# Performance work log

Hardware: AMD Instinct MI355X
Metric: run time of the kernel (lower is better)

Reference implementation:

```python
import jax, jax.numpy as jnp
import numpy as np

DT = 0.05      # bsde.delta_t
EPS = 1e-6     # BatchNormalization epsilon


def _bn(x, gamma, beta):
    # training-mode batch norm: statistics over the batch axis
    m = jnp.mean(x, axis=0, keepdims=True)
    v = jnp.var(x, axis=0, keepdims=True)
    return (x - m) * jax.lax.rsqrt(v + EPS) * gamma + beta


def _subnet(x, g0, b0, W0, g1, b1, W1, g2, b2, W2, bias2, g3, b3):
    # bn -> (dense -> bn -> relu) x 2 -> dense(+bias) -> bn
    x = _bn(x, g0, b0)
    x = jax.nn.relu(_bn(x @ W0, g1, b1))
    x = jax.nn.relu(_bn(x @ W1, g2, b2))
    x = _bn(x @ W2 + bias2, g3, b3)
    return x


def setup_inputs() -> dict:
    key = jax.random.key(0)
    B, D, N, H = 8192, 100, 20, 110
    T = N - 1  # number of subnets
    ks = jax.random.split(key, 18)
    u = lambda k, s, lo, hi: jax.random.uniform(k, s, jnp.float32, lo, hi)
    s_dh = np.sqrt(2.0 / (D + H)).astype(np.float32)
    s_hh = np.sqrt(2.0 / (H + H)).astype(np.float32)
    s_hd = np.sqrt(2.0 / (H + D)).astype(np.float32)
    return {
        "dw": jax.random.normal(ks[0], (B, D, N), jnp.float32) * np.sqrt(DT).astype(np.float32),
        "x": jax.random.normal(ks[1], (B, D, N + 1), jnp.float32),
        "mean_y_input": jax.random.normal(ks[2], (N,), jnp.float32),
        "y_init": u(ks[3], (1,), 0.0, 1.0),
        "z_init": u(ks[4], (1, D), -0.1, 0.1),
        "gamma0": u(ks[5], (T, D), 0.1, 0.5),
        "beta0": 0.1 * jax.random.normal(ks[6], (T, D), jnp.float32),
        "W0": s_dh * jax.random.normal(ks[7], (T, D, H), jnp.float32),
        "gamma1": u(ks[8], (T, H), 0.1, 0.5),
        "beta1": 0.1 * jax.random.normal(ks[9], (T, H), jnp.float32),
        "W1": s_hh * jax.random.normal(ks[10], (T, H, H), jnp.float32),
        "gamma2": u(ks[11], (T, H), 0.1, 0.5),
        "beta2": 0.1 * jax.random.normal(ks[12], (T, H), jnp.float32),
        "W2": s_hd * jax.random.normal(ks[13], (T, H, D), jnp.float32),
        "bias2": jnp.zeros((T, D), jnp.float32),
        "gamma3": u(ks[14], (T, D), 0.1, 0.5),
        "beta3": 0.1 * jax.random.normal(ks[15], (T, D), jnp.float32),
    }


def reference(dw, x, mean_y_input, y_init, z_init, gamma0, beta0, W0,
              gamma1, beta1, W1, gamma2, beta2, W2, bias2, gamma3, beta3):
    B, D, N = dw.shape
    T = N - 1
    # z at step t+1 depends only on x[:, :, t+1] and subnet t -> compute all in parallel
    x_steps = jnp.moveaxis(x[:, :, 1:N], 2, 0)  # [T, B, D]
    z_all = jax.vmap(_subnet)(x_steps, gamma0, beta0, W0, gamma1, beta1, W1,
                              gamma2, beta2, W2, bias2, gamma3, beta3) / D  # [T, B, D]
    z0 = jnp.broadcast_to(z_init, (B, D))          # all_one_vec @ z_init
    zs = jnp.concatenate([z0[None], z_all], axis=0)  # [N, B, D] (z used at each update)
    dw_steps = jnp.moveaxis(dw, 2, 0)               # [N, B, D]
    y0 = jnp.ones((B, 1), dw.dtype) * y_init

    def step(y, zd):
        z, dwt = zd
        # f_tf(t, x, y, z) = sin(y) for the SineBM equation
        y_new = y - DT * jnp.sin(y) + jnp.sum(z * dwt, axis=1, keepdims=True)
        return y_new, jnp.mean(y_new)

    y_final, means = jax.lax.scan(step, y0, (zs, dw_steps))
    mean_y = jnp.concatenate([jnp.mean(y0)[None], means[:T]])  # length N
    return y_final, mean_y
```

## Files before the change

kernel.cpp:

```cpp
#include <hip/hip_runtime.h>

typedef unsigned short u16;
typedef unsigned int   u32;

#define BATCH  8192
#define DIM    100
#define HID    110
#define TSUB   19
#define NSTEP  20
#define KP     128
#define NPAD   112
#define BN_EPS 1e-6f
#define DT_C   0.05f

#define SAB  1024
#define SAR  (BATCH / SAB)
#define SLICES 32

#define A3P  101

typedef __bf16 v8bf __attribute__((ext_vector_type(8)));
typedef float  v4f  __attribute__((ext_vector_type(4)));
typedef u16    u16x4 __attribute__((ext_vector_type(4)));

__device__ __forceinline__ u16 f2bf(float f) {
    u32 u = __float_as_uint(f);
    return (u16)((u + 0x7fffu + ((u >> 16) & 1u)) >> 16);
}
__device__ __forceinline__ float bf2f(u16 h) {
    return __uint_as_float(((u32)h) << 16);
}
__device__ __forceinline__ void acc4(float4& s, float4& q, float4 v) {
    s.x += v.x; s.y += v.y; s.z += v.z; s.w += v.w;
    q.x += v.x * v.x; q.y += v.y * v.y; q.z += v.z * v.z; q.w += v.w * v.w;
}

__global__ void statsA(const float* __restrict__ x, float* __restrict__ part,
                       u32* __restrict__ xT32) {
    __shared__ u16 xls[SAR][2112];
    const int tid = threadIdx.x;
    const int b0 = blockIdx.x * SAR;
    float4 s0 = {0,0,0,0}, q0 = {0,0,0,0};
    float4 s1 = {0,0,0,0}, q1 = {0,0,0,0};
    float4 s2 = {0,0,0,0}, q2 = {0,0,0,0};
#pragma unroll
    for (int r = 0; r < SAR; r++) {
        const float4* row = (const float4*)(x + (size_t)(b0 + r) * 2100);
        float4 v0 = row[tid];
        float4 v1 = row[tid + 256];
        acc4(s0, q0, v0);
        acc4(s1, q1, v1);
        u16x4 p0 = { f2bf(v0.x), f2bf(v0.y), f2bf(v0.z), f2bf(v0.w) };
        u16x4 p1 = { f2bf(v1.x), f2bf(v1.y), f2bf(v1.z), f2bf(v1.w) };
        *(u16x4*)&xls[r][tid * 4]        = p0;
        *(u16x4*)&xls[r][1024 + tid * 4] = p1;
        if (tid < 13) {
            float4 v2 = row[tid + 512];
            acc4(s2, q2, v2);
            u16x4 p2 = { f2bf(v2.x), f2bf(v2.y), f2bf(v2.z), f2bf(v2.w) };
            *(u16x4*)&xls[r][2048 + tid * 4] = p2;
        }
    }
    float* ps = part + (size_t)blockIdx.x * 4200;
    *(float4*)&ps[tid * 4]               = s0;
    *(float4*)&ps[1024 + tid * 4]        = s1;
    *(float4*)&ps[2100 + tid * 4]        = q0;
    *(float4*)&ps[2100 + 1024 + tid * 4] = q1;
    if (tid < 13) {
        *(float4*)&ps[2048 + tid * 4]        = s2;
        *(float4*)&ps[2100 + 2048 + tid * 4] = q2;
    }
    __syncthreads();
    const int TOT = TSUB * SAR * (NPAD / 2);
    for (int i = tid; i < TOT; i += 256) {
        int w = i % (NPAD / 2);
        int seg = i / (NPAD / 2);
        int r = seg % SAR, t = seg / SAR;
        int d0 = w * 2;
        u32 v = 0;
        if (d0 < DIM) {
            u16 lo = xls[r][d0 * 21 + t + 1];
            u16 hi = (d0 + 1 < DIM) ? xls[r][(d0 + 1) * 21 + t + 1] : (u16)0;
            v = (u32)lo | ((u32)hi << 16);
        }
        xT32[((size_t)t * BATCH + b0 + r) * (NPAD / 2) + w] = v;
    }
}

__global__ void statsB(const float* __restrict__ part, float* __restrict__ out) {
    int gid = blockIdx.x * 256 + threadIdx.x;
    if (gid >= 4200 * SLICES) return;
    int slice = gid / 4200;
    int o = gid - slice * 4200;
    const float* p = part + (size_t)slice * (SAB / SLICES) * 4200 + o;
    float acc = 0.f;
#pragma unroll 4
    for (int i = 0; i < SAB / SLICES; i++) acc += p[(size_t)i * 4200];
    atomicAdd(&out[o], acc);
}

__global__ void wtrans(const float* __restrict__ W0, const float* __restrict__ W1,
                       const float* __restrict__ W2, u16* __restrict__ WTsw) {
    __shared__ float lw[HID * HID];
    const int t = blockIdx.x, l = blockIdx.y, tid = threadIdx.x;
    const float* W; int K, N;
    if (l == 0)      { W = W0; K = DIM; N = HID; }
    else if (l == 1) { W = W1; K = HID; N = HID; }
    else             { W = W2; K = HID; N = DIM; }
    const float* Wt = W + (size_t)t * K * N;
    for (int i = tid; i < K * N; i += 256) lw[i] = Wt[i];
    __syncthreads();
    u16* out = WTsw + ((size_t)l * TSUB + t) * (NPAD * KP);
    for (int i = tid; i < NPAD * 16; i += 256) {
        int n = i / 16, p = i % 16;
        int kc = p ^ (n & 7);
        u16 o8[8];
#pragma unroll
        for (int j = 0; j < 8; j++) {
            int k = kc * 8 + j;
            float v = (k < K && n < N) ? lw[k * N + n] : 0.f;
            o8[j] = f2bf(v);
        }
        *(uint4*)&out[(size_t)n * KP + p * 8] = *(uint4*)o8;
    }
}

template <int KREAL, int NOUT, int IDXMODE, int RELU>
__global__ void gemm_kernel(const u16* __restrict__ Ain,
                            const u16* __restrict__ WTswL,
                            const float* __restrict__ sumIn,
                            const float* __restrict__ sqIn,
                            const float* __restrict__ gIn,
                            const float* __restrict__ bIn,
                            u16* __restrict__ Hout,
                            float* __restrict__ sumArr,
                            float* __restrict__ sqArr) {
    __shared__ __align__(16) u16 Alds[128 * KP];
    __shared__ __align__(16) u16 Blds[NPAD * KP];
    __shared__ float s_sum[NPAD], s_sq[NPAD];
    __shared__ float aAffL[KP], cAffL[KP];

    const int tid = threadIdx.x;
    const int mt = blockIdx.x;
    const int t  = blockIdx.y;
    const int brow0 = mt * 128;

    if (tid < NPAD) { s_sum[tid] = 0.f; s_sq[tid] = 0.f; }
    if (tid < KREAL) {
        int idx = (IDXMODE == 0) ? (tid * 21 + (t + 1)) : (t * KREAL + tid);
        float m = sumIn[idx] * (1.f / BATCH);
        float v = sqIn[idx] * (1.f / BATCH) - m * m;
        float rstd = rsqrtf(v + BN_EPS);
        float ga = gIn[t * KREAL + tid] * rstd;
        aAffL[tid] = ga;
        cAffL[tid] = bIn[t * KREAL + tid] - m * ga;
    }

    {
        const uint4* wsrc = (const uint4*)(WTswL + (size_t)t * NPAD * KP);
        uint4* bl = (uint4*)Blds;
#pragma unroll
        for (int i = 0; i < 7; i++) bl[tid + i * 256] = wsrc[tid + i * 256];
    }
    const int NCH = (KREAL + 7) / 8;
    for (int i = tid; i < 128 * (16 - NCH); i += 256) {
        int row = i / (16 - NCH);
        int kc  = NCH + i % (16 - NCH);
        uint4 z = {0, 0, 0, 0};
        *(uint4*)&Alds[row * KP + (kc ^ (row & 7)) * 8] = z;
    }
    __syncthreads();

    for (int cidx = tid; cidx < 128 * NCH; cidx += 256) {
        int row = cidx / NCH;
        int kc  = cidx % NCH;
        int k0  = kc * 8;
        const u16* hrow = Ain + ((size_t)t * BATCH + brow0 + row) * NPAD + k0;
        u16 hv[8];
        *(uint4*)hv = *(const uint4*)hrow;
        u16 pk[8];
#pragma unroll
        for (int j = 0; j < 8; j++) {
            int k = k0 + j;
            float av = (k < KREAL) ? fmaf(bf2f(hv[j]), aAffL[k], cAffL[k]) : 0.f;
            if (RELU) av = fmaxf(av, 0.f);
            pk[j] = f2bf(av);
        }
        *(uint4*)&Alds[row * KP + ((kc ^ (row & 7)) * 8)] = *(uint4*)pk;
    }
    __syncthreads();

    const int lane = tid & 63;
    const int wv   = tid >> 6;
    const int r0   = lane & 15;
    const int q    = lane >> 4;
    const int moff = wv * 32;

    v4f acc[2][7];
#pragma unroll
    for (int i = 0; i < 2; i++)
#pragma unroll
        for (int j = 0; j < 7; j++) { v4f z = {0.f, 0.f, 0.f, 0.f}; acc[i][j] = z; }

#pragma unroll
    for (int ks = 0; ks < 4; ks++) {
        int cbase = ks * 4 + q;
        v8bf afr[2];
#pragma unroll
        for (int mf = 0; mf < 2; mf++) {
            int row = moff + mf * 16 + r0;
            afr[mf] = *(const v8bf*)&Alds[row * KP + ((cbase ^ (row & 7)) * 8)];
        }
#pragma unroll
        for (int nf = 0; nf < 7; nf++) {
            int nr = nf * 16 + r0;
            v8bf bfr = *(const v8bf*)&Blds[nr * KP + ((cbase ^ (nr & 7)) * 8)];
            acc[0][nf] = __builtin_amdgcn_mfma_f32_16x16x32_bf16(afr[0], bfr, acc[0][nf], 0, 0, 0);
            acc[1][nf] = __builtin_amdgcn_mfma_f32_16x16x32_bf16(afr[1], bfr, acc[1][nf], 0, 0, 0);
        }
    }

#pragma unroll
    for (int mf = 0; mf < 2; mf++) {
#pragma unroll
        for (int nf = 0; nf < 7; nf++) {
            int n = nf * 16 + r0;
#pragma unroll
            for (int rg = 0; rg < 4; rg++) {
                int grow = brow0 + moff + mf * 16 + q * 4 + rg;
                Hout[((size_t)t * BATCH + grow) * NPAD + n] = f2bf(acc[mf][nf][rg]);
            }
        }
    }
#pragma unroll
    for (int nf = 0; nf < 7; nf++) {
        float cs = 0.f, cq = 0.f;
#pragma unroll
        for (int mf = 0; mf < 2; mf++)
#pragma unroll
            for (int rg = 0; rg < 4; rg++) {
                float vv = acc[mf][nf][rg];
                cs += vv; cq += vv * vv;
            }
        cs += __shfl_xor(cs, 16); cs += __shfl_xor(cs, 32);
        cq += __shfl_xor(cq, 16); cq += __shfl_xor(cq, 32);
        if (q == 0) {
            atomicAdd(&s_sum[nf * 16 + r0], cs);
            atomicAdd(&s_sq[nf * 16 + r0], cq);
        }
    }
    __syncthreads();
    if (tid < NOUT) {
        atomicAdd(&sumArr[t * NOUT + tid], s_sum[tid]);
        atomicAdd(&sqArr[t * NOUT + tid], s_sq[tid]);
    }
}

__global__ __launch_bounds__(256, 4)
void scan_kernel(const float* __restrict__ dw,
                 const u16* __restrict__ zbuf,
                 const float* __restrict__ sum3, const float* __restrict__ sq3,
                 const float* __restrict__ g3, const float* __restrict__ b3,
                 const float* __restrict__ z_init, const float* __restrict__ y_init,
                 float* __restrict__ yout, float* __restrict__ meanout) {
    __shared__ float a3l[TSUB * A3P], c3l[TSUB * A3P];
    __shared__ float bsum[NSTEP];
    const int tid = threadIdx.x;
    for (int i = tid; i < TSUB * DIM; i += 256) {
        int t = i / DIM, d = i - t * DIM;
        float m = sum3[i] * (1.f / BATCH);
        float v = sq3[i] * (1.f / BATCH) - m * m;
        float rstd = rsqrtf(v + BN_EPS);
        float ga = g3[i] * rstd;
        a3l[t * A3P + d] = ga * (1.f / DIM);
        c3l[t * A3P + d] = (b3[i] - m * ga) * (1.f / DIM);
    }
    if (tid < NSTEP) bsum[tid] = 0.f;
    __syncthreads();

    const int wv = tid >> 6, lane = tid & 63;
    const int b = blockIdx.x * 4 + wv;

    v4f w[10];
    u32 zr[TSUB];
    float zi0 = 0.f, zi1 = 0.f;
    if (lane < 50) {
        const v4f* dwb4 = (const v4f*)(dw + (size_t)b * (DIM * NSTEP) + lane * 40);
#pragma unroll
        for (int j = 0; j < 10; j++) w[j] = dwb4[j];
#pragma unroll
        for (int t = 0; t < TSUB; t++)
            zr[t] = *(const u32*)(zbuf + ((size_t)t * BATCH + b) * NPAD + 2 * lane);
        float2 zi = *(const float2*)(z_init + 2 * lane);
        zi0 = zi.x; zi1 = zi.y;
#pragma unroll
        for (int j = 0; j < 10; j++) asm volatile("" :: "v"(w[j]));
#pragma unroll
        for (int t = 0; t < TSUB; t++) asm volatile("" :: "v"(zr[t]));
    }

    float acc[NSTEP];
#pragma unroll
    for (int k = 0; k < NSTEP; k++) acc[k] = 0.f;
    if (lane < 50) {
        const int dbase = 2 * lane;
        acc[0] = zi0 * w[0][0] + zi1 * w[5][0];
#pragma unroll
        for (int t = 0; t < TSUB; t++) {
            float a0 = a3l[t * A3P + dbase],     c0 = c3l[t * A3P + dbase];
            float a1 = a3l[t * A3P + dbase + 1], c1 = c3l[t * A3P + dbase + 1];
            u32 z = zr[t];
            float za0 = fmaf(bf2f((u16)(z & 0xffffu)), a0, c0);
            float za1 = fmaf(bf2f((u16)(z >> 16)),     a1, c1);
            const int n = t + 1, j = n >> 2, k = n & 3;
            acc[n] += w[j][k] * za0 + w[5 + j][k] * za1;
        }
    }

#pragma unroll
    for (int m = 1; m < 64; m <<= 1) {
#pragma unroll
        for (int k = 0; k < NSTEP; k++) acc[k] += __shfl_xor(acc[k], m, 64);
    }

    const float yi = y_init[0];
    float y = yi, ysave = 0.f;
#pragma unroll
    for (int i = 0; i < NSTEP; i++) {
        y = y - DT_C * __sinf(y) + acc[i];
        if (i == lane - 1) ysave = y;
    }
    if (lane == 0) yout[b] = y;
    if (lane >= 1 && lane < NSTEP) atomicAdd(&bsum[lane], ysave);
    __syncthreads();
    if (tid >= 1 && tid < NSTEP) atomicAdd(&meanout[tid], bsum[tid] * (1.f / BATCH));
    if (blockIdx.x == 0 && tid == 0) meanout[0] = yi;
}

extern "C" void kernel_launch(void* const* d_in, const int* in_sizes, int n_in,
                              void* d_out, int out_size, void* d_ws, size_t ws_size,
                              hipStream_t stream) {
    const float* dw     = (const float*)d_in[0];
    const float* x      = (const float*)d_in[1];
    const float* y_init = (const float*)d_in[3];
    const float* z_init = (const float*)d_in[4];
    const float* g0 = (const float*)d_in[5];
    const float* b0 = (const float*)d_in[6];
    const float* W0 = (const float*)d_in[7];
    const float* g1 = (const float*)d_in[8];
    const float* b1 = (const float*)d_in[9];
    const float* W1 = (const float*)d_in[10];
    const float* g2 = (const float*)d_in[11];
    const float* b2 = (const float*)d_in[12];
    const float* W2 = (const float*)d_in[13];
    const float* g3 = (const float*)d_in[15];
    const float* b3 = (const float*)d_in[16];

    char* ws = (char*)d_ws;
    size_t off = 0;
    auto alloc = [&](size_t bytes) -> void* {
        off = (off + 255) & ~(size_t)255;
        void* p = ws + off;
        off += bytes;
        return p;
    };

    const int nStats = 4200 + TSUB * HID * 2 * 2 + TSUB * DIM * 2;
    float* statsBlk = (float*)alloc((size_t)nStats * 4);
    float* sum0 = statsBlk;            float* sq0  = sum0 + 2100;
    float* sum1 = sum0 + 4200;         float* sq1  = sum1 + TSUB * HID;
    float* sum2 = sq1 + TSUB * HID;    float* sq2  = sum2 + TSUB * HID;
    float* sum3 = sq2 + TSUB * HID;    float* sq3  = sum3 + TSUB * DIM;

    u16* WTsw = (u16*)alloc((size_t)3 * TSUB * NPAD * KP * 2);

    const size_t hBytes = (size_t)TSUB * BATCH * NPAD * 2;
    u16* h0 = (u16*)alloc(hBytes);
    u16* h1 = (u16*)alloc(hBytes);
    u16* outbuf = h0;
    float* part = (float*)h0;
    u32*  xT32  = (u32*)h1;

    float* yout = (float*)d_out;
    float* meanout = yout + BATCH;

    hipMemsetAsync(statsBlk, 0, (size_t)nStats * 4, stream);
    hipMemsetAsync(meanout, 0, NSTEP * 4, stream);

    wtrans<<<dim3(TSUB, 3), 256, 0, stream>>>(W0, W1, W2, WTsw);
    statsA<<<SAB, 256, 0, stream>>>(x, part, xT32);
    statsB<<<(4200 * SLICES + 255) / 256, 256, 0, stream>>>(part, sum0);

    const u16* xT = (const u16*)xT32;
    u16* WT0 = WTsw;
    u16* WT1 = WTsw + (size_t)TSUB * NPAD * KP;
    u16* WT2 = WTsw + (size_t)2 * TSUB * NPAD * KP;

    gemm_kernel<DIM, HID, 0, 0><<<dim3(64, TSUB), 256, 0, stream>>>(xT, WT0, sum0, sq0, g0, b0, h0, sum1, sq1);
    gemm_kernel<HID, HID, 1, 1><<<dim3(64, TSUB), 256, 0, stream>>>(h0, WT1, sum1, sq1, g1, b1, h1, sum2, sq2);
    gemm_kernel<HID, DIM, 1, 1><<<dim3(64, TSUB), 256, 0, stream>>>(h1, WT2, sum2, sq2, g2, b2, outbuf, sum3, sq3);

    scan_kernel<<<2048, 256, 0, stream>>>(dw, outbuf, sum3, sq3, g3, b3, z_init, y_init, yout, meanout);
}
```

Baseline: 194.1 us.

## Store final GEMM output batch-major and issue scan loads via inline asm

The last GEMM now writes its output batch-major ([B][T][NPAD]), so each scan wave reads all 19 subnet z values for one batch row from a contiguous region instead of 19 strided locations. The scan kernel issues its dw, z and z_init loads as explicit inline-asm global loads with immediate offsets, clamping inactive lanes to a valid address so the loads need no branch. It then waits once for all loads to complete. Launch bounds occupancy drops from 4 to 3 to give the kernel more registers. The GEMM stores become more scattered in exchange, and the hand-written asm loads bypass the compiler's scheduling.

```diff
diff --git a/kernel.cpp b/kernel.cpp
--- a/kernel.cpp
+++ b/kernel.cpp
@@ -21,6 +21,7 @@
 
 typedef __bf16 v8bf __attribute__((ext_vector_type(8)));
 typedef float  v4f  __attribute__((ext_vector_type(4)));
+typedef float  v2f  __attribute__((ext_vector_type(2)));
 typedef u16    u16x4 __attribute__((ext_vector_type(4)));
 
 __device__ __forceinline__ u16 f2bf(float f) {
@@ -125,7 +126,7 @@
     }
 }
 
-template <int KREAL, int NOUT, int IDXMODE, int RELU>
+template <int KREAL, int NOUT, int IDXMODE, int RELU, int BMAJOR>
 __global__ void gemm_kernel(const u16* __restrict__ Ain,
                             const u16* __restrict__ WTswL,
                             const float* __restrict__ sumIn,
@@ -228,7 +229,9 @@
 #pragma unroll
             for (int rg = 0; rg < 4; rg++) {
                 int grow = brow0 + moff + mf * 16 + q * 4 + rg;
-                Hout[((size_t)t * BATCH + grow) * NPAD + n] = f2bf(acc[mf][nf][rg]);
+                size_t oidx = BMAJOR ? ((size_t)grow * (TSUB * NPAD) + (size_t)t * NPAD + n)
+                                     : (((size_t)t * BATCH + grow) * NPAD + n);
+                Hout[oidx] = f2bf(acc[mf][nf][rg]);
             }
         }
     }
@@ -256,7 +259,7 @@
     }
 }
 
-__global__ __launch_bounds__(256, 4)
+__global__ __launch_bounds__(256, 3)
 void scan_kernel(const float* __restrict__ dw,
                  const u16* __restrict__ zbuf,
                  const float* __restrict__ sum3, const float* __restrict__ sq3,
@@ -280,23 +283,32 @@
 
     const int wv = tid >> 6, lane = tid & 63;
     const int b = blockIdx.x * 4 + wv;
+    const int ll = (lane < 50) ? lane : 49;
 
     v4f w[10];
     u32 zr[TSUB];
-    float zi0 = 0.f, zi1 = 0.f;
-    if (lane < 50) {
-        const v4f* dwb4 = (const v4f*)(dw + (size_t)b * (DIM * NSTEP) + lane * 40);
-#pragma unroll
-        for (int j = 0; j < 10; j++) w[j] = dwb4[j];
+    v2f zi;
+    {
+        const float* dwaddr = dw + (size_t)b * (DIM * NSTEP) + ll * 40;
+        const u16*   zaddr  = zbuf + (size_t)b * (TSUB * NPAD) + 2 * ll;
+        const float* ziaddr = z_init + 2 * ll;
+        asm volatile("global_load_dwordx4 %0, %1, off offset:0"   : "=v"(w[0]) : "v"(dwaddr));
+        asm volatile("global_load_dwordx4 %0, %1, off offset:16"  : "=v"(w[1]) : "v"(dwaddr));
+        asm volatile("global_load_dwordx4 %0, %1, off offset:32"  : "=v"(w[2]) : "v"(dwaddr));
+        asm volatile("global_load_dwordx4 %0, %1, off offset:48"  : "=v"(w[3]) : "v"(dwaddr));
+        asm volatile("global_load_dwordx4 %0, %1, off offset:64"  : "=v"(w[4]) : "v"(dwaddr));
+        asm volatile("global_load_dwordx4 %0, %1, off offset:80"  : "=v"(w[5]) : "v"(dwaddr));
+        asm volatile("global_load_dwordx4 %0, %1, off offset:96"  : "=v"(w[6]) : "v"(dwaddr));
+        asm volatile("global_load_dwordx4 %0, %1, off offset:112" : "=v"(w[7]) : "v"(dwaddr));
+        asm volatile("global_load_dwordx4 %0, %1, off offset:128" : "=v"(w[8]) : "v"(dwaddr));
+        asm volatile("global_load_dwordx4 %0, %1, off offset:144" : "=v"(w[9]) : "v"(dwaddr));
 #pragma unroll
         for (int t = 0; t < TSUB; t++)
-            zr[t] = *(const u32*)(zbuf + ((size_t)t * BATCH + b) * NPAD + 2 * lane);
-        float2 zi = *(const float2*)(z_init + 2 * lane);
-        zi0 = zi.x; zi1 = zi.y;
-#pragma unroll
-        for (int j = 0; j < 10; j++) asm volatile("" :: "v"(w[j]));
-#pragma unroll
-        for (int t = 0; t < TSUB; t++) asm volatile("" :: "v"(zr[t]));
+            asm volatile("global_load_dword %0, %1, off offset:%2"
+                         : "=v"(zr[t]) : "v"(zaddr), "i"(t * NPAD * 2));
+        asm volatile("global_load_dwordx2 %0, %1, off" : "=v"(zi) : "v"(ziaddr));
+        asm volatile("s_waitcnt vmcnt(0)" ::: "memory");
+        __builtin_amdgcn_sched_barrier(0);
     }
 
     float acc[NSTEP];
@@ -304,7 +316,7 @@
     for (int k = 0; k < NSTEP; k++) acc[k] = 0.f;
     if (lane < 50) {
         const int dbase = 2 * lane;
-        acc[0] = zi0 * w[0][0] + zi1 * w[5][0];
+        acc[0] = zi[0] * w[0][0] + zi[1] * w[5][0];
 #pragma unroll
         for (int t = 0; t < TSUB; t++) {
             float a0 = a3l[t * A3P + dbase],     c0 = c3l[t * A3P + dbase];
@@ -396,9 +408,9 @@
     u16* WT1 = WTsw + (size_t)TSUB * NPAD * KP;
     u16* WT2 = WTsw + (size_t)2 * TSUB * NPAD * KP;
 
-    gemm_kernel<DIM, HID, 0, 0><<<dim3(64, TSUB), 256, 0, stream>>>(xT, WT0, sum0, sq0, g0, b0, h0, sum1, sq1);
-    gemm_kernel<HID, HID, 1, 1><<<dim3(64, TSUB), 256, 0, stream>>>(h0, WT1, sum1, sq1, g1, b1, h1, sum2, sq2);
-    gemm_kernel<HID, DIM, 1, 1><<<dim3(64, TSUB), 256, 0, stream>>>(h1, WT2, sum2, sq2, g2, b2, outbuf, sum3, sq3);
+    gemm_kernel<DIM, HID, 0, 0, 0><<<dim3(64, TSUB), 256, 0, stream>>>(xT, WT0, sum0, sq0, g0, b0, h0, sum1, sq1);
+    gemm_kernel<HID, HID, 1, 1, 0><<<dim3(64, TSUB), 256, 0, stream>>>(h0, WT1, sum1, sq1, g1, b1, h1, sum2, sq2);
+    gemm_kernel<HID, DIM, 1, 1, 1><<<dim3(64, TSUB), 256, 0, stream>>>(h1, WT2, sum2, sq2, g2, b2, outbuf, sum3, sq3);
 
     scan_kernel<<<2048, 256, 0, stream>>>(dw, outbuf, sum3, sq3, g3, b3, z_init, y_init, yout, meanout);
 }
```

After: 195.6 us. No clear change (+0.8%).
